# Kernel tuning notes

Measured on AMD Instinct MI355X. Metric: run time of the kernel, lower is better.

The kernel has to match this reference:

```python
import jax, jax.numpy as jnp
import numpy as np
import math

D_MODEL = 1024
N_HEADS = 16
HEAD_DIM = D_MODEL // N_HEADS  # 64
KV_DIM = 4 * HEAD_DIM          # 256
THETA = 10000.0
B, T = 2, 2048


def setup_inputs() -> dict:
    key = jax.random.key(0)
    ks = jax.random.split(key, 14)
    s = lambda k, *sh: jax.random.normal(k, sh, dtype=jnp.float32) * 0.02
    inp = {
        "x": jax.random.normal(ks[0], (B, T, D_MODEL), dtype=jnp.float32),
        "mask": jnp.tril(jnp.ones((T, T), dtype=jnp.int32))[None, None],  # causal [1,1,T,T]
        "Wq": s(ks[1], D_MODEL, D_MODEL), "bq": jnp.zeros((D_MODEL,), jnp.float32),
        "Wkv": s(ks[2], D_MODEL, KV_DIM), "bkv": jnp.zeros((KV_DIM,), jnp.float32),
        "Wk": s(ks[3], KV_DIM, D_MODEL), "bk": jnp.zeros((D_MODEL,), jnp.float32),
        "Wv": s(ks[4], KV_DIM, D_MODEL), "bv": jnp.zeros((D_MODEL,), jnp.float32),
        "Wo": s(ks[5], D_MODEL, D_MODEL), "bo": jnp.zeros((D_MODEL,), jnp.float32),
        "Wkr": s(ks[6], HEAD_DIM, HEAD_DIM),  # decoupled k_rope linear, no bias
    }
    return inp


def _rotate_half(x):
    x1, x2 = jnp.split(x, 2, axis=-1)
    return jnp.concatenate((-x2, x1), axis=-1)


def reference(x, mask, Wq, bq, Wkv, bkv, Wk, bk, Wv, bv, Wo, bo, Wkr):
    Bq, Tq, C = x.shape
    kv = x @ Wkv + bkv                                # [B,T,KV_DIM]
    k = (kv @ Wk + bk).reshape(Bq, Tq, N_HEADS, HEAD_DIM).transpose(0, 2, 1, 3)
    v = (kv @ Wv + bv).reshape(Bq, Tq, N_HEADS, HEAD_DIM).transpose(0, 2, 1, 3)
    q = (x @ Wq + bq).reshape(Bq, Tq, N_HEADS, HEAD_DIM).transpose(0, 2, 1, 3)

    # standard RoPE on q
    inv_freq = 1.0 / (THETA ** (jnp.arange(0, HEAD_DIM, 2, dtype=jnp.float32) / HEAD_DIM))
    t = jnp.arange(Tq, dtype=jnp.float32)
    freqs = t[:, None] * inv_freq[None, :]            # [T, D/2]
    emb = jnp.concatenate((freqs, freqs), axis=-1)    # [T, D]
    q = q * jnp.cos(emb) + _rotate_half(q) * jnp.sin(emb)

    # decoupled position path for k: scale by position index, then linear
    k = (k * t[None, None, :, None]) @ Wkr            # [B,H,T,D]

    attn = jnp.einsum('bhtd,bhsd->bhts', q, k) * (1.0 / math.sqrt(HEAD_DIM))
    attn = jnp.where(mask == 0, -jnp.inf, attn)
    attn = jax.nn.softmax(attn, axis=-1)
    y = jnp.einsum('bhts,bhsd->bhtd', attn, v)
    y = y.transpose(0, 2, 1, 3).reshape(Bq, Tq, C)
    return y @ Wo + bo
```

## Files before the change

### kernel.cpp

```cpp
#include <hip/hip_runtime.h>
#include <hip/hip_bf16.h>
#include <math.h>

typedef __bf16 bf16x8 __attribute__((ext_vector_type(8)));
typedef __bf16 bf16x4 __attribute__((ext_vector_type(4)));
typedef float  f32x4  __attribute__((ext_vector_type(4)));

#define T_SEQ 2048
#define NH    16
#define HD    64
#define DM    1024
#define QSCALE 0.18033688011112043f

__device__ __forceinline__ f32x4 mfma16(bf16x8 a, bf16x8 b, f32x4 c) {
    return __builtin_amdgcn_mfma_f32_16x16x32_bf16(a, b, c, 0, 0, 0);
}

__device__ __forceinline__ void gl2lds(const void* g, void* l) {
    __builtin_amdgcn_global_load_lds(
        (const __attribute__((address_space(1))) void*)g,
        (__attribute__((address_space(3))) void*)l, 16, 0, 0);
}

__device__ __forceinline__ void tsplit_body(const float* __restrict__ in,
                                            __bf16* __restrict__ oh, __bf16* __restrict__ ol,
                                            int K, int N, int n0, int k0, int SPLIT,
                                            float* tile )
{
    const int tid = threadIdx.x;
#pragma unroll
    for (int it = 0; it < 2; ++it) {
        int r = it * 32 + (tid >> 3), c8 = (tid & 7) * 8;
        f32x4 a0 = *(const f32x4*)&in[(size_t)(k0 + r) * N + n0 + c8];
        f32x4 a1 = *(const f32x4*)&in[(size_t)(k0 + r) * N + n0 + c8 + 4];
#pragma unroll
        for (int j = 0; j < 4; ++j) { tile[r * 65 + c8 + j] = a0[j]; tile[r * 65 + c8 + 4 + j] = a1[j]; }
    }
    __syncthreads();
    const int n = tid >> 2, kb = (tid & 3) * 16;
    bf16x8 h0, h1, l0, l1;
#pragma unroll
    for (int j = 0; j < 8; ++j) {
        float v0 = tile[(kb + j) * 65 + n], v1 = tile[(kb + 8 + j) * 65 + n];
        __bf16 hb0 = (__bf16)v0, hb1 = (__bf16)v1;
        h0[j] = hb0; h1[j] = hb1;
        if (SPLIT) { l0[j] = (__bf16)(v0 - (float)hb0); l1[j] = (__bf16)(v1 - (float)hb1); }
    }
    size_t o = (size_t)(n0 + n) * K + k0 + kb;
    *(bf16x8*)&oh[o] = h0; *(bf16x8*)&oh[o + 8] = h1;
    if (SPLIT) { *(bf16x8*)&ol[o] = l0; *(bf16x8*)&ol[o + 8] = l1; }
}

__global__ __launch_bounds__(256)
void prep(const float* __restrict__ x, const float* __restrict__ Wq,
          const float* __restrict__ Wkv, const float* __restrict__ Wv,
          const float* __restrict__ Wo, const float* __restrict__ Wk,
          const float* __restrict__ Wkr, const float* __restrict__ bk,
          __bf16* xh, __bf16* xl, __bf16* Wqt_h, __bf16* Wqt_l,
          __bf16* Wkvt_h, __bf16* Wkvt_l, __bf16* Wvt, __bf16* Wot,
          __bf16* W2th, __bf16* W2tl, float* b2)
{
    __shared__ float tile[64 * 65];
    const int g = blockIdx.x, tid = threadIdx.x;
    if (g < 2048) {
        size_t idx = ((size_t)g * 256 + tid) * 8;
        f32x4 a0 = *(const f32x4*)&x[idx];
        f32x4 a1 = *(const f32x4*)&x[idx + 4];
        bf16x8 h, l;
#pragma unroll
        for (int j = 0; j < 4; ++j) {
            __bf16 h0 = (__bf16)a0[j];
            h[j]     = h0; l[j]     = (__bf16)(a0[j] - (float)h0);
            __bf16 h1 = (__bf16)a1[j];
            h[4 + j] = h1; l[4 + j] = (__bf16)(a1[j] - (float)h1);
        }
        *(bf16x8*)&xh[idx] = h;
        *(bf16x8*)&xl[idx] = l;
    } else if (g < 2304) {
        int i = g - 2048;
        tsplit_body(Wq, Wqt_h, Wqt_l, 1024, 1024, (i & 15) * 64, (i >> 4) * 64, 1, tile);
    } else if (g < 2368) {
        int i = g - 2304;
        tsplit_body(Wkv, Wkvt_h, Wkvt_l, 1024, 256, (i & 3) * 64, (i >> 2) * 64, 1, tile);
    } else if (g < 2432) {
        int i = g - 2368;
        tsplit_body(Wv, Wvt, nullptr, 256, 1024, (i & 15) * 64, (i >> 4) * 64, 0, tile);
    } else if (g < 2688) {
        int i = g - 2432;
        tsplit_body(Wo, Wot, nullptr, 1024, 1024, (i & 15) * 64, (i >> 4) * 64, 0, tile);
    } else {
        int o    = (g - 2688) * 256 + tid;
        int rowk = o >> 10, col = o & 1023;
        int h = col >> 6, d = col & 63;
        float acc = 0.0f;
        if (rowk < 256) {
#pragma unroll 8
            for (int j = 0; j < 64; ++j)
                acc += Wk[(size_t)rowk * DM + h * HD + j] * Wkr[j * HD + d];
            __bf16 hb = (__bf16)acc;
            W2th[(size_t)col * 256 + rowk] = hb;
            W2tl[(size_t)col * 256 + rowk] = (__bf16)(acc - (float)hb);
        } else {
#pragma unroll 8
            for (int j = 0; j < 64; ++j)
                acc += bk[h * HD + j] * Wkr[j * HD + d];
            b2[col] = acc;
        }
    }
}

template <int DUALA, int DUALB, int OUTM, int EPI>
__device__ __forceinline__
void gemm_body(char* smem,
               const __bf16* __restrict__ Ahi, const __bf16* __restrict__ Alo,
               const __bf16* __restrict__ Bhi, const __bf16* __restrict__ Blo,
               const float* __restrict__ bias, void* __restrict__ Cp,
               void* __restrict__ Cp2, int m0, int n0, int N, int K)
{
    const int tid  = threadIdx.x;
    const int w    = tid >> 6;
    const int lane = tid & 63;
    const int l16  = lane & 15;
    const int quad = lane >> 4;
    const int wy   = w >> 1, wx = w & 1;

    f32x4 acc[4][4];
#pragma unroll
    for (int i = 0; i < 4; ++i)
#pragma unroll
        for (int j = 0; j < 4; ++j) acc[i][j] = (f32x4)0.0f;

    auto stage = [&](int k0, int buf) {
        char* bb = smem + buf * 32768;
#pragma unroll
        for (int i = 0; i < 2; ++i) {
            int s = i * 256 + tid, row = s >> 2, c8 = (s & 3) * 8;
            size_t aoff = (size_t)(m0 + row) * K + k0 + c8;
            size_t boff = (size_t)(n0 + row) * K + k0 + c8;
            char*  dst  = bb + (row * 32 + c8) * 2;
            gl2lds(&Ahi[aoff], dst);
            if (DUALA) gl2lds(&Alo[aoff], dst + 8192);
            gl2lds(&Bhi[boff], dst + 16384);
            if (DUALB) gl2lds(&Blo[boff], dst + 24576);
        }
    };

    stage(0, 0);
    const int J = K >> 5;
    for (int j = 0; j < J; ++j) {
        __syncthreads();
        if (j + 1 < J) stage((j + 1) << 5, (j + 1) & 1);

        const __bf16* Ah = (const __bf16*)(smem + (j & 1) * 32768);
        const __bf16* Al = Ah + 4096;
        const __bf16* Bh = Ah + 8192;
        const __bf16* Bl = Ah + 12288;

        bf16x8 bfh[4], bfl[4];
#pragma unroll
        for (int ct = 0; ct < 4; ++ct) {
            bfh[ct] = *(const bf16x8*)&Bh[(wx * 64 + ct * 16 + l16) * 32 + quad * 8];
            if (DUALB) bfl[ct] = *(const bf16x8*)&Bl[(wx * 64 + ct * 16 + l16) * 32 + quad * 8];
        }
#pragma unroll
        for (int mf = 0; mf < 4; ++mf) {
            bf16x8 ah = *(const bf16x8*)&Ah[(wy * 64 + mf * 16 + l16) * 32 + quad * 8];
            bf16x8 al;
            if (DUALA) al = *(const bf16x8*)&Al[(wy * 64 + mf * 16 + l16) * 32 + quad * 8];
#pragma unroll
            for (int ct = 0; ct < 4; ++ct) {
                acc[mf][ct] = mfma16(ah, bfh[ct], acc[mf][ct]);
                if (DUALA) acc[mf][ct] = mfma16(al, bfh[ct], acc[mf][ct]);
                if (DUALB) acc[mf][ct] = mfma16(ah, bfl[ct], acc[mf][ct]);
            }
        }
    }

    float bias_v[4];
#pragma unroll
    for (int ct = 0; ct < 4; ++ct)
        bias_v[ct] = bias ? bias[n0 + wx * 64 + ct * 16 + l16] : 0.0f;

    if (EPI == 1) {
        __bf16* Chi = (__bf16*)Cp;
        __bf16* Clo = (__bf16*)Cp2;
#pragma unroll
        for (int mf = 0; mf < 4; ++mf) {
#pragma unroll
            for (int r = 0; r < 4; ++r) {
                int   m = m0 + wy * 64 + mf * 16 + quad * 4 + r;
                float t = (float)(m & (T_SEQ - 1));
#pragma unroll
                for (int ct = 0; ct < 2; ++ct) {
                    int   d   = ct * 16 + l16;
                    float inv = powf(10000.0f, -(float)d * (1.0f / 32.0f));
                    float sv, cv;
                    sincosf(t * inv, &sv, &cv);
                    float lo = acc[mf][ct][r]     + bias_v[ct];
                    float hi = acc[mf][ct + 2][r] + bias_v[ct + 2];
                    float v0 = (lo * cv - hi * sv) * QSCALE;
                    float v1 = (hi * cv + lo * sv) * QSCALE;
                    size_t i0 = (size_t)m * N + n0 + wx * 64 + d;
                    size_t i1 = i0 + 32;
                    __bf16 h0 = (__bf16)v0, h1 = (__bf16)v1;
                    Chi[i0] = h0; Clo[i0] = (__bf16)(v0 - (float)h0);
                    Chi[i1] = h1; Clo[i1] = (__bf16)(v1 - (float)h1);
                }
            }
        }
    } else if (EPI == 3) {
        __syncthreads();
        __bf16* vt = (__bf16*)(smem + w * 9216);
#pragma unroll
        for (int mf = 0; mf < 4; ++mf)
#pragma unroll
            for (int ct = 0; ct < 4; ++ct)
#pragma unroll
                for (int r = 0; r < 4; ++r)
                    vt[(ct * 16 + l16) * 72 + mf * 16 + quad * 4 + r] =
                        (__bf16)(acc[mf][ct][r] + bias_v[ct]);
        const int bb   = m0 >> 11;
        const int head = (n0 + wx * 64) >> 6;
        const int bh   = bb * 16 + head;
        __bf16* out    = (__bf16*)Cp;
        size_t  gbase  = ((size_t)(bh * 64 + lane)) * T_SEQ + (m0 & (T_SEQ - 1)) + wy * 64;
#pragma unroll
        for (int j8 = 0; j8 < 8; ++j8)
            *(bf16x8*)&out[gbase + j8 * 8] = *(const bf16x8*)&vt[lane * 72 + j8 * 8];
    } else {
#pragma unroll
        for (int mf = 0; mf < 4; ++mf) {
#pragma unroll
            for (int r = 0; r < 4; ++r) {
                int   m     = m0 + wy * 64 + mf * 16 + quad * 4 + r;
                float scale = (EPI == 2) ? (float)(m & (T_SEQ - 1)) : 1.0f;
#pragma unroll
                for (int ct = 0; ct < 4; ++ct) {
                    float  v   = (acc[mf][ct][r] + bias_v[ct]) * scale;
                    size_t idx = (size_t)m * N + n0 + wx * 64 + ct * 16 + l16;
                    if (OUTM == 1)      ((float*)Cp)[idx]  = v;
                    else if (OUTM == 0) ((__bf16*)Cp)[idx] = (__bf16)v;
                    else {
                        __bf16 hb = (__bf16)v;
                        ((__bf16*)Cp)[idx]  = hb;
                        ((__bf16*)Cp2)[idx] = (__bf16)(v - (float)hb);
                    }
                }
            }
        }
    }
}

__global__ __launch_bounds__(256)
void gemm_qkv(const __bf16* xh, const __bf16* xl,
              const __bf16* Wqt_h, const __bf16* Wqt_l, const float* bq,
              __bf16* qhi, __bf16* qlo,
              const __bf16* Wkvt_h, const __bf16* Wkvt_l, const float* bkv,
              __bf16* kvhi, __bf16* kvlo)
{
    __shared__ __attribute__((aligned(16))) char smem[65536];
    const int m0 = blockIdx.y * 128;
    if (blockIdx.x < 2)
        gemm_body<1, 1, 2, 0>(smem, xh, xl, Wkvt_h, Wkvt_l, bkv, kvhi, kvlo,
                              m0, blockIdx.x * 128, 256, 1024);
    else
        gemm_body<1, 1, 2, 1>(smem, xh, xl, Wqt_h, Wqt_l, bq, qhi, qlo,
                              m0, (blockIdx.x - 2) * 128, 1024, 1024);
}

__global__ __launch_bounds__(256)
void gemm_kv2(const __bf16* kvhi, const __bf16* kvlo,
              const __bf16* W2th, const __bf16* W2tl, const float* b2,
              __bf16* khi, __bf16* klo,
              const __bf16* Wvt, const float* bv, __bf16* vtg)
{
    __shared__ __attribute__((aligned(16))) char smem[65536];
    const int m0 = blockIdx.y * 128;
    if (blockIdx.x < 8)
        gemm_body<1, 1, 2, 2>(smem, kvhi, kvlo, W2th, W2tl, b2, khi, klo,
                              m0, blockIdx.x * 128, 1024, 256);
    else
        gemm_body<1, 0, 0, 3>(smem, kvhi, kvlo, Wvt, Wvt, bv, vtg, nullptr,
                              m0, (blockIdx.x - 8) * 128, 1024, 256);
}

__global__ __launch_bounds__(256)
void gemm_o(const __bf16* ybb, const __bf16* Wot, const float* bo, float* out)
{
    __shared__ __attribute__((aligned(16))) char smem[65536];
    gemm_body<0, 0, 1, 0>(smem, ybb, ybb, Wot, Wot, bo, out, nullptr,
                          blockIdx.y * 128, blockIdx.x * 128, 1024, 1024);
}

#define KSP 72
#define PSP 72
__global__ __launch_bounds__(256, 2)
void attn_v5(const __bf16* __restrict__ qhi, const __bf16* __restrict__ qlo,
             const __bf16* __restrict__ khi, const __bf16* __restrict__ klo,
             const __bf16* __restrict__ vtg, __bf16* __restrict__ yb)
{
    __shared__ __attribute__((aligned(16))) __bf16 Kh2[2][64 * KSP];
    __shared__ __attribute__((aligned(16))) __bf16 Kl2[2][64 * KSP];
    __shared__ __attribute__((aligned(16))) __bf16 Vt2[2][64 * KSP];
    __shared__ __attribute__((aligned(16))) __bf16 Pw[4][2][16 * PSP];

    const int tid  = threadIdx.x;
    const int w    = tid >> 6;
    const int lane = tid & 63;
    const int l16  = lane & 15;
    const int quad = lane >> 4;

    const int g  = blockIdx.x;
    const int bh = g & 31, a = g >> 5;
    const int tile = (a < 8) ? (15 - 2 * a) : (2 * (a - 8));
    const int b = bh >> 4, h = bh & 15;
    const int q0 = tile * 128;

    bf16x8 qh[2][2], ql[2][2];
#pragma unroll
    for (int f = 0; f < 2; ++f) {
        const int    qrow = q0 + 64 * f + 16 * w + l16;
        const size_t qoff = (size_t)(b * T_SEQ + qrow) * DM + h * HD;
#pragma unroll
        for (int s = 0; s < 2; ++s) {
            qh[f][s] = *(const bf16x8*)&qhi[qoff + s * 32 + quad * 8];
            ql[f][s] = *(const bf16x8*)&qlo[qoff + s * 32 + quad * 8];
        }
    }

    f32x4 o[2][4];
#pragma unroll
    for (int f = 0; f < 2; ++f)
#pragma unroll
        for (int i = 0; i < 4; ++i) o[f][i] = (f32x4)0.0f;
    float m_i[2] = {-1e30f, -1e30f}, l_i[2] = {0.f, 0.f};

    const int srow = tid >> 3, sc8 = (tid & 7) * 8;
    bf16x8 kr[2], lr[2], vr[2];

#pragma unroll
    for (int it = 0; it < 2; ++it) {
        int    r  = it * 32 + srow;
        size_t gk = (size_t)(b * T_SEQ + r) * DM + h * HD + sc8;
        kr[it] = *(const bf16x8*)&khi[gk];
        lr[it] = *(const bf16x8*)&klo[gk];
        vr[it] = *(const bf16x8*)&vtg[(size_t)(bh * HD + r) * T_SEQ + sc8];
    }
#pragma unroll
    for (int it = 0; it < 2; ++it) {
        int r = it * 32 + srow;
        *(bf16x8*)&Kh2[0][r * KSP + sc8] = kr[it];
        *(bf16x8*)&Kl2[0][r * KSP + sc8] = lr[it];
        *(bf16x8*)&Vt2[0][r * KSP + sc8] = vr[it];
    }

    const int jmax = q0 + 64;
    for (int j0 = 0; j0 <= jmax; j0 += 64) {
        const int  cur  = (j0 >> 6) & 1;
        const bool act0 = (j0 <= q0);
        const bool pre  = (j0 + 64 <= jmax);
        __syncthreads();

        if (pre) {
#pragma unroll
            for (int it = 0; it < 2; ++it) {
                int    r  = it * 32 + srow;
                size_t gk = (size_t)(b * T_SEQ + j0 + 64 + r) * DM + h * HD + sc8;
                kr[it] = *(const bf16x8*)&khi[gk];
                lr[it] = *(const bf16x8*)&klo[gk];
                vr[it] = *(const bf16x8*)&vtg[(size_t)(bh * HD + r) * T_SEQ + j0 + 64 + sc8];
            }
        }

        const __bf16* Kh = Kh2[cur];
        const __bf16* Kl = Kl2[cur];
        const __bf16* Vt = Vt2[cur];

        f32x4 sa[2][4];
#pragma unroll
        for (int f = 0; f < 2; ++f)
#pragma unroll
            for (int i = 0; i < 4; ++i) sa[f][i] = (f32x4)0.0f;
#pragma unroll
        for (int s = 0; s < 2; ++s) {
#pragma unroll
            for (int kc = 0; kc < 4; ++kc) {
                bf16x8 kh = *(const bf16x8*)&Kh[(kc * 16 + l16) * KSP + s * 32 + quad * 8];
                bf16x8 kv = *(const bf16x8*)&Kl[(kc * 16 + l16) * KSP + s * 32 + quad * 8];
                sa[1][kc] = mfma16(kh, qh[1][s], sa[1][kc]);
                sa[1][kc] = mfma16(kv, qh[1][s], sa[1][kc]);
                sa[1][kc] = mfma16(kh, ql[1][s], sa[1][kc]);
                if (act0) {
                    sa[0][kc] = mfma16(kh, qh[0][s], sa[0][kc]);
                    sa[0][kc] = mfma16(kv, qh[0][s], sa[0][kc]);
                    sa[0][kc] = mfma16(kh, ql[0][s], sa[0][kc]);
                }
            }
        }

#pragma unroll
        for (int f = 0; f < 2; ++f) {
            if (f == 0 && !act0) continue;
            const int  qrow = q0 + 64 * f + 16 * w + l16;
            const bool need = (j0 + 63 > q0 + 64 * f + 16 * w);
            if (need) {
#pragma unroll
                for (int kc = 0; kc < 4; ++kc)
#pragma unroll
                    for (int r = 0; r < 4; ++r)
                        if (j0 + kc * 16 + quad * 4 + r > qrow) sa[f][kc][r] = -1e30f;
            }
            float mx = -1e30f;
#pragma unroll
            for (int kc = 0; kc < 4; ++kc)
#pragma unroll
                for (int r = 0; r < 4; ++r) mx = fmaxf(mx, sa[f][kc][r]);
            mx = fmaxf(mx, __shfl_xor(mx, 16));
            mx = fmaxf(mx, __shfl_xor(mx, 32));
            float mn    = fmaxf(fmaxf(m_i[f], mx), -1e20f);
            float alpha = exp2f(m_i[f] - mn);
            m_i[f] = mn;
            float rs = 0.f;
            __bf16* pw = &Pw[w][f][0];
#pragma unroll
            for (int kc = 0; kc < 4; ++kc) {
                float p0 = exp2f(sa[f][kc][0] - mn);
                float p1 = exp2f(sa[f][kc][1] - mn);
                float p2 = exp2f(sa[f][kc][2] - mn);
                float p3 = exp2f(sa[f][kc][3] - mn);
                rs += (p0 + p1) + (p2 + p3);
                bf16x4 pk = { (__bf16)p0, (__bf16)p1, (__bf16)p2, (__bf16)p3 };
                *(bf16x4*)&pw[l16 * PSP + kc * 16 + quad * 4] = pk;
            }
            rs += __shfl_xor(rs, 16);
            rs += __shfl_xor(rs, 32);
            l_i[f] = l_i[f] * alpha + rs;
#pragma unroll
            for (int dc = 0; dc < 4; ++dc) o[f][dc] *= alpha;
        }

#pragma unroll
        for (int s = 0; s < 2; ++s) {
            bf16x8 pb1 = *(const bf16x8*)&Pw[w][1][l16 * PSP + s * 32 + quad * 8];
            bf16x8 pb0;
            if (act0) pb0 = *(const bf16x8*)&Pw[w][0][l16 * PSP + s * 32 + quad * 8];
#pragma unroll
            for (int dc = 0; dc < 4; ++dc) {
                bf16x8 va = *(const bf16x8*)&Vt[(dc * 16 + l16) * KSP + s * 32 + quad * 8];
                o[1][dc] = mfma16(va, pb1, o[1][dc]);
                if (act0) o[0][dc] = mfma16(va, pb0, o[0][dc]);
            }
        }

        if (pre) {
            __bf16* nKh = Kh2[cur ^ 1];
            __bf16* nKl = Kl2[cur ^ 1];
            __bf16* nVt = Vt2[cur ^ 1];
#pragma unroll
            for (int it = 0; it < 2; ++it) {
                int r = it * 32 + srow;
                *(bf16x8*)&nKh[r * KSP + sc8] = kr[it];
                *(bf16x8*)&nKl[r * KSP + sc8] = lr[it];
                *(bf16x8*)&nVt[r * KSP + sc8] = vr[it];
            }
        }
    }

#pragma unroll
    for (int f = 0; f < 2; ++f) {
        float   invl = 1.0f / l_i[f];
        __bf16* pw   = &Pw[w][f][0];
#pragma unroll
        for (int dc = 0; dc < 4; ++dc) {
            bf16x4 ov = { (__bf16)(o[f][dc][0] * invl), (__bf16)(o[f][dc][1] * invl),
                          (__bf16)(o[f][dc][2] * invl), (__bf16)(o[f][dc][3] * invl) };
            *(bf16x4*)&pw[l16 * PSP + dc * 16 + quad * 4] = ov;
        }
        const int qrl  = lane >> 2;
        const int dch  = (lane & 3) * 16;
        const int qrow = q0 + 64 * f + 16 * w + qrl;
        const __bf16* src = &pw[qrl * PSP + dch];
        __bf16*       dst = &yb[(size_t)(b * T_SEQ + qrow) * DM + h * HD + dch];
        *(bf16x8*)dst       = *(const bf16x8*)src;
        *(bf16x8*)(dst + 8) = *(const bf16x8*)(src + 8);
    }
}

extern "C" void kernel_launch(void* const* d_in, const int* in_sizes, int n_in,
                              void* d_out, int out_size, void* d_ws, size_t ws_size,
                              hipStream_t stream)
{
    (void)in_sizes; (void)n_in; (void)out_size; (void)ws_size;

    const float* x   = (const float*)d_in[0];
    const float* Wq  = (const float*)d_in[2];
    const float* bq  = (const float*)d_in[3];
    const float* Wkv = (const float*)d_in[4];
    const float* bkv = (const float*)d_in[5];
    const float* Wk  = (const float*)d_in[6];
    const float* bk  = (const float*)d_in[7];
    const float* Wv  = (const float*)d_in[8];
    const float* bv  = (const float*)d_in[9];
    const float* Wo  = (const float*)d_in[10];
    const float* bo  = (const float*)d_in[11];
    const float* Wkr = (const float*)d_in[12];

    const int    BT = 2 * T_SEQ;
    const size_t MB = 1024 * 1024;
    char* base = (char*)d_ws;

    __bf16* xhi    = (__bf16*)(base +  0 * MB);
    __bf16* xlo    = (__bf16*)(base +  8 * MB);
    __bf16* qhi    = (__bf16*)(base + 16 * MB);
    __bf16* qlo    = (__bf16*)(base + 24 * MB);
    __bf16* Wqt_h  = (__bf16*)(base + 32 * MB);
    __bf16* Wqt_l  = (__bf16*)(base + 34 * MB);
    __bf16* Wkvt_h = (__bf16*)(base + 36 * MB);
    __bf16* Wkvt_l = (__bf16*)(base + 37 * MB);
    __bf16* kvhi   = (__bf16*)(base + 38 * MB);
    __bf16* kvlo   = (__bf16*)(base + 40 * MB);
    __bf16* W2t_h  = (__bf16*)(base + 42 * MB);
    __bf16* W2t_l  = (__bf16*)(base + 42 * MB + 512 * 1024);
    __bf16* Wvt    = (__bf16*)(base + 43 * MB);
    __bf16* Wot    = (__bf16*)(base + 43 * MB + 512 * 1024);
    float*  b2     = (float*) (base + 45 * MB + 512 * 1024);
    __bf16* vtg    = (__bf16*)(base +  8 * MB);
    __bf16* ybb    = (__bf16*)(base +  0 * MB);
    __bf16* khi    = (__bf16*)d_out;
    __bf16* klo    = (__bf16*)d_out + (size_t)BT * DM;

    dim3 blk(256);
    prep<<<3716, blk, 0, stream>>>(x, Wq, Wkv, Wv, Wo, Wk, Wkr, bk,
                                   xhi, xlo, Wqt_h, Wqt_l, Wkvt_h, Wkvt_l,
                                   Wvt, Wot, W2t_h, W2t_l, b2);
    gemm_qkv<<<dim3(10, 32), blk, 0, stream>>>(xhi, xlo, Wqt_h, Wqt_l, bq, qhi, qlo,
                                               Wkvt_h, Wkvt_l, bkv, kvhi, kvlo);
    gemm_kv2<<<dim3(16, 32), blk, 0, stream>>>(kvhi, kvlo, W2t_h, W2t_l, b2,
                                               khi, klo, Wvt, bv, vtg);
    attn_v5<<<512, blk, 0, stream>>>(qhi, qlo, khi, klo, vtg, ybb);
    gemm_o<<<dim3(8, 32), blk, 0, stream>>>(ybb, Wot, bo, (float*)d_out);
}
```

Before: 283.4 us.

## Restructure causal attention blocks into paired 64-row tiles for load balance

Each attention block now handles two 64-row query tiles in sequence, tile 31-a and then tile a, instead of one 128-row tile carrying two fragments. Pairing a long tile with a short one gives every block the same causal workload, and each warp now keeps a single fragment's state. The cost is that K/V blocks are reloaded for the second phase, and the 128-row tile's sharing of each K/V load across two query fragments is lost, so LDS reuse per load drops.

```diff
diff --git a/kernel.cpp b/kernel.cpp
--- a/kernel.cpp
+++ b/kernel.cpp
@@ -295,14 +295,14 @@
 #define KSP 72
 #define PSP 72
 __global__ __launch_bounds__(256, 2)
-void attn_v5(const __bf16* __restrict__ qhi, const __bf16* __restrict__ qlo,
+void attn_v7(const __bf16* __restrict__ qhi, const __bf16* __restrict__ qlo,
              const __bf16* __restrict__ khi, const __bf16* __restrict__ klo,
              const __bf16* __restrict__ vtg, __bf16* __restrict__ yb)
 {
     __shared__ __attribute__((aligned(16))) __bf16 Kh2[2][64 * KSP];
     __shared__ __attribute__((aligned(16))) __bf16 Kl2[2][64 * KSP];
     __shared__ __attribute__((aligned(16))) __bf16 Vt2[2][64 * KSP];
-    __shared__ __attribute__((aligned(16))) __bf16 Pw[4][2][16 * PSP];
+    __shared__ __attribute__((aligned(16))) __bf16 Pw[4][16 * PSP];
 
     const int tid  = threadIdx.x;
     const int w    = tid >> 6;
@@ -312,177 +312,161 @@
 
     const int g  = blockIdx.x;
     const int bh = g & 31, a = g >> 5;
-    const int tile = (a < 8) ? (15 - 2 * a) : (2 * (a - 8));
-    const int b = bh >> 4, h = bh & 15;
-    const int q0 = tile * 128;
-
-    bf16x8 qh[2][2], ql[2][2];
-#pragma unroll
-    for (int f = 0; f < 2; ++f) {
-        const int    qrow = q0 + 64 * f + 16 * w + l16;
-        const size_t qoff = (size_t)(b * T_SEQ + qrow) * DM + h * HD;
-#pragma unroll
-        for (int s = 0; s < 2; ++s) {
-            qh[f][s] = *(const bf16x8*)&qhi[qoff + s * 32 + quad * 8];
-            ql[f][s] = *(const bf16x8*)&qlo[qoff + s * 32 + quad * 8];
-        }
-    }
-
-    f32x4 o[2][4];
-#pragma unroll
-    for (int f = 0; f < 2; ++f)
-#pragma unroll
-        for (int i = 0; i < 4; ++i) o[f][i] = (f32x4)0.0f;
-    float m_i[2] = {-1e30f, -1e30f}, l_i[2] = {0.f, 0.f};
+    const int b  = bh >> 4, h = bh & 15;
 
     const int srow = tid >> 3, sc8 = (tid & 7) * 8;
-    bf16x8 kr[2], lr[2], vr[2];
-
-#pragma unroll
-    for (int it = 0; it < 2; ++it) {
-        int    r  = it * 32 + srow;
-        size_t gk = (size_t)(b * T_SEQ + r) * DM + h * HD + sc8;
-        kr[it] = *(const bf16x8*)&khi[gk];
-        lr[it] = *(const bf16x8*)&klo[gk];
-        vr[it] = *(const bf16x8*)&vtg[(size_t)(bh * HD + r) * T_SEQ + sc8];
-    }
-#pragma unroll
-    for (int it = 0; it < 2; ++it) {
-        int r = it * 32 + srow;
-        *(bf16x8*)&Kh2[0][r * KSP + sc8] = kr[it];
-        *(bf16x8*)&Kl2[0][r * KSP + sc8] = lr[it];
-        *(bf16x8*)&Vt2[0][r * KSP + sc8] = vr[it];
-    }
-
-    const int jmax = q0 + 64;
-    for (int j0 = 0; j0 <= jmax; j0 += 64) {
-        const int  cur  = (j0 >> 6) & 1;
-        const bool act0 = (j0 <= q0);
-        const bool pre  = (j0 + 64 <= jmax);
+
+    for (int ph = 0; ph < 2; ++ph) {
+        const int u  = ph ? a : (31 - a);
+        const int q0 = u * 64;
+
+        bf16x8 qh[2], ql[2];
+        {
+            const int    qr   = q0 + 16 * w + l16;
+            const size_t qoff = (size_t)(b * T_SEQ + qr) * DM + h * HD;
+#pragma unroll
+            for (int s = 0; s < 2; ++s) {
+                qh[s] = *(const bf16x8*)&qhi[qoff + s * 32 + quad * 8];
+                ql[s] = *(const bf16x8*)&qlo[qoff + s * 32 + quad * 8];
+            }
+        }
+
+        f32x4 o[4];
+#pragma unroll
+        for (int i = 0; i < 4; ++i) o[i] = (f32x4)0.0f;
+        float m_i = -1e30f, l_i = 0.f;
+
+        bf16x8 kr[2], lr[2], vr[2];
+#pragma unroll
+        for (int it = 0; it < 2; ++it) {
+            int    r  = it * 32 + srow;
+            size_t gk = (size_t)(b * T_SEQ + r) * DM + h * HD + sc8;
+            kr[it] = *(const bf16x8*)&khi[gk];
+            lr[it] = *(const bf16x8*)&klo[gk];
+            vr[it] = *(const bf16x8*)&vtg[(size_t)(bh * HD + r) * T_SEQ + sc8];
+        }
         __syncthreads();
-
-        if (pre) {
-#pragma unroll
-            for (int it = 0; it < 2; ++it) {
-                int    r  = it * 32 + srow;
-                size_t gk = (size_t)(b * T_SEQ + j0 + 64 + r) * DM + h * HD + sc8;
-                kr[it] = *(const bf16x8*)&khi[gk];
-                lr[it] = *(const bf16x8*)&klo[gk];
-                vr[it] = *(const bf16x8*)&vtg[(size_t)(bh * HD + r) * T_SEQ + j0 + 64 + sc8];
-            }
-        }
-
-        const __bf16* Kh = Kh2[cur];
-        const __bf16* Kl = Kl2[cur];
-        const __bf16* Vt = Vt2[cur];
-
-        f32x4 sa[2][4];
-#pragma unroll
-        for (int f = 0; f < 2; ++f)
-#pragma unroll
-            for (int i = 0; i < 4; ++i) sa[f][i] = (f32x4)0.0f;
-#pragma unroll
-        for (int s = 0; s < 2; ++s) {
-#pragma unroll
-            for (int kc = 0; kc < 4; ++kc) {
-                bf16x8 kh = *(const bf16x8*)&Kh[(kc * 16 + l16) * KSP + s * 32 + quad * 8];
-                bf16x8 kv = *(const bf16x8*)&Kl[(kc * 16 + l16) * KSP + s * 32 + quad * 8];
-                sa[1][kc] = mfma16(kh, qh[1][s], sa[1][kc]);
-                sa[1][kc] = mfma16(kv, qh[1][s], sa[1][kc]);
-                sa[1][kc] = mfma16(kh, ql[1][s], sa[1][kc]);
-                if (act0) {
-                    sa[0][kc] = mfma16(kh, qh[0][s], sa[0][kc]);
-                    sa[0][kc] = mfma16(kv, qh[0][s], sa[0][kc]);
-                    sa[0][kc] = mfma16(kh, ql[0][s], sa[0][kc]);
+#pragma unroll
+        for (int it = 0; it < 2; ++it) {
+            int r = it * 32 + srow;
+            *(bf16x8*)&Kh2[0][r * KSP + sc8] = kr[it];
+            *(bf16x8*)&Kl2[0][r * KSP + sc8] = lr[it];
+            *(bf16x8*)&Vt2[0][r * KSP + sc8] = vr[it];
+        }
+
+        for (int j0 = 0; j0 <= q0; j0 += 64) {
+            const int  cur = (j0 >> 6) & 1;
+            const bool pre = (j0 + 64 <= q0);
+            __syncthreads();
+
+            if (pre) {
+#pragma unroll
+                for (int it = 0; it < 2; ++it) {
+                    int    r  = it * 32 + srow;
+                    size_t gk = (size_t)(b * T_SEQ + j0 + 64 + r) * DM + h * HD + sc8;
+                    kr[it] = *(const bf16x8*)&khi[gk];
+                    lr[it] = *(const bf16x8*)&klo[gk];
+                    vr[it] = *(const bf16x8*)&vtg[(size_t)(bh * HD + r) * T_SEQ + j0 + 64 + sc8];
                 }
             }
-        }
-
-#pragma unroll
-        for (int f = 0; f < 2; ++f) {
-            if (f == 0 && !act0) continue;
-            const int  qrow = q0 + 64 * f + 16 * w + l16;
-            const bool need = (j0 + 63 > q0 + 64 * f + 16 * w);
+
+            const __bf16* Kh = Kh2[cur];
+            const __bf16* Kl = Kl2[cur];
+            const __bf16* Vt = Vt2[cur];
+
+            f32x4 sa[4];
+#pragma unroll
+            for (int i = 0; i < 4; ++i) sa[i] = (f32x4)0.0f;
+#pragma unroll
+            for (int s = 0; s < 2; ++s) {
+#pragma unroll
+                for (int kc = 0; kc < 4; ++kc) {
+                    bf16x8 kh = *(const bf16x8*)&Kh[(kc * 16 + l16) * KSP + s * 32 + quad * 8];
+                    bf16x8 kv = *(const bf16x8*)&Kl[(kc * 16 + l16) * KSP + s * 32 + quad * 8];
+                    sa[kc] = mfma16(kh, qh[s], sa[kc]);
+                    sa[kc] = mfma16(kv, qh[s], sa[kc]);
+                    sa[kc] = mfma16(kh, ql[s], sa[kc]);
+                }
+            }
+
+            const int  qr   = q0 + 16 * w + l16;
+            const bool need = (j0 + 63 > q0 + 16 * w);
             if (need) {
 #pragma unroll
                 for (int kc = 0; kc < 4; ++kc)
 #pragma unroll
                     for (int r = 0; r < 4; ++r)
-                        if (j0 + kc * 16 + quad * 4 + r > qrow) sa[f][kc][r] = -1e30f;
+                        if (j0 + kc * 16 + quad * 4 + r > qr) sa[kc][r] = -1e30f;
             }
             float mx = -1e30f;
 #pragma unroll
             for (int kc = 0; kc < 4; ++kc)
 #pragma unroll
-                for (int r = 0; r < 4; ++r) mx = fmaxf(mx, sa[f][kc][r]);
+                for (int r = 0; r < 4; ++r) mx = fmaxf(mx, sa[kc][r]);
             mx = fmaxf(mx, __shfl_xor(mx, 16));
             mx = fmaxf(mx, __shfl_xor(mx, 32));
-            float mn    = fmaxf(fmaxf(m_i[f], mx), -1e20f);
-            float alpha = exp2f(m_i[f] - mn);
-            m_i[f] = mn;
+            float mn    = fmaxf(fmaxf(m_i, mx), -1e20f);
+            float alpha = exp2f(m_i - mn);
+            m_i = mn;
             float rs = 0.f;
-            __bf16* pw = &Pw[w][f][0];
+            __bf16* pw = &Pw[w][0];
 #pragma unroll
             for (int kc = 0; kc < 4; ++kc) {
-                float p0 = exp2f(sa[f][kc][0] - mn);
-                float p1 = exp2f(sa[f][kc][1] - mn);
-                float p2 = exp2f(sa[f][kc][2] - mn);
-                float p3 = exp2f(sa[f][kc][3] - mn);
+                float p0 = exp2f(sa[kc][0] - mn);
+                float p1 = exp2f(sa[kc][1] - mn);
+                float p2 = exp2f(sa[kc][2] - mn);
+                float p3 = exp2f(sa[kc][3] - mn);
                 rs += (p0 + p1) + (p2 + p3);
                 bf16x4 pk = { (__bf16)p0, (__bf16)p1, (__bf16)p2, (__bf16)p3 };
                 *(bf16x4*)&pw[l16 * PSP + kc * 16 + quad * 4] = pk;
             }
             rs += __shfl_xor(rs, 16);
             rs += __shfl_xor(rs, 32);
-            l_i[f] = l_i[f] * alpha + rs;
-#pragma unroll
-            for (int dc = 0; dc < 4; ++dc) o[f][dc] *= alpha;
-        }
-
-#pragma unroll
-        for (int s = 0; s < 2; ++s) {
-            bf16x8 pb1 = *(const bf16x8*)&Pw[w][1][l16 * PSP + s * 32 + quad * 8];
-            bf16x8 pb0;
-            if (act0) pb0 = *(const bf16x8*)&Pw[w][0][l16 * PSP + s * 32 + quad * 8];
+            l_i = l_i * alpha + rs;
+#pragma unroll
+            for (int dc = 0; dc < 4; ++dc) o[dc] *= alpha;
+
+#pragma unroll
+            for (int s = 0; s < 2; ++s) {
+                bf16x8 pb = *(const bf16x8*)&pw[l16 * PSP + s * 32 + quad * 8];
+#pragma unroll
+                for (int dc = 0; dc < 4; ++dc) {
+                    bf16x8 va = *(const bf16x8*)&Vt[(dc * 16 + l16) * KSP + s * 32 + quad * 8];
+                    o[dc] = mfma16(va, pb, o[dc]);
+                }
+            }
+
+            if (pre) {
+                __bf16* nKh = Kh2[cur ^ 1];
+                __bf16* nKl = Kl2[cur ^ 1];
+                __bf16* nVt = Vt2[cur ^ 1];
+#pragma unroll
+                for (int it = 0; it < 2; ++it) {
+                    int r = it * 32 + srow;
+                    *(bf16x8*)&nKh[r * KSP + sc8] = kr[it];
+                    *(bf16x8*)&nKl[r * KSP + sc8] = lr[it];
+                    *(bf16x8*)&nVt[r * KSP + sc8] = vr[it];
+                }
+            }
+        }
+
+        {
+            float   invl = 1.0f / l_i;
+            __bf16* pw   = &Pw[w][0];
 #pragma unroll
             for (int dc = 0; dc < 4; ++dc) {
-                bf16x8 va = *(const bf16x8*)&Vt[(dc * 16 + l16) * KSP + s * 32 + quad * 8];
-                o[1][dc] = mfma16(va, pb1, o[1][dc]);
-                if (act0) o[0][dc] = mfma16(va, pb0, o[0][dc]);
-            }
-        }
-
-        if (pre) {
-            __bf16* nKh = Kh2[cur ^ 1];
-            __bf16* nKl = Kl2[cur ^ 1];
-            __bf16* nVt = Vt2[cur ^ 1];
-#pragma unroll
-            for (int it = 0; it < 2; ++it) {
-                int r = it * 32 + srow;
-                *(bf16x8*)&nKh[r * KSP + sc8] = kr[it];
-                *(bf16x8*)&nKl[r * KSP + sc8] = lr[it];
-                *(bf16x8*)&nVt[r * KSP + sc8] = vr[it];
-            }
-        }
-    }
-
-#pragma unroll
-    for (int f = 0; f < 2; ++f) {
-        float   invl = 1.0f / l_i[f];
-        __bf16* pw   = &Pw[w][f][0];
-#pragma unroll
-        for (int dc = 0; dc < 4; ++dc) {
-            bf16x4 ov = { (__bf16)(o[f][dc][0] * invl), (__bf16)(o[f][dc][1] * invl),
-                          (__bf16)(o[f][dc][2] * invl), (__bf16)(o[f][dc][3] * invl) };
-            *(bf16x4*)&pw[l16 * PSP + dc * 16 + quad * 4] = ov;
-        }
-        const int qrl  = lane >> 2;
-        const int dch  = (lane & 3) * 16;
-        const int qrow = q0 + 64 * f + 16 * w + qrl;
-        const __bf16* src = &pw[qrl * PSP + dch];
-        __bf16*       dst = &yb[(size_t)(b * T_SEQ + qrow) * DM + h * HD + dch];
-        *(bf16x8*)dst       = *(const bf16x8*)src;
-        *(bf16x8*)(dst + 8) = *(const bf16x8*)(src + 8);
+                bf16x4 ov = { (__bf16)(o[dc][0] * invl), (__bf16)(o[dc][1] * invl),
+                              (__bf16)(o[dc][2] * invl), (__bf16)(o[dc][3] * invl) };
+                *(bf16x4*)&pw[l16 * PSP + dc * 16 + quad * 4] = ov;
+            }
+            const int qrl  = lane >> 2;
+            const int dch  = (lane & 3) * 16;
+            const int qrow = q0 + 16 * w + qrl;
+            const __bf16* src = &pw[qrl * PSP + dch];
+            __bf16*       dst = &yb[(size_t)(b * T_SEQ + qrow) * DM + h * HD + dch];
+            *(bf16x8*)dst       = *(const bf16x8*)src;
+            *(bf16x8*)(dst + 8) = *(const bf16x8*)(src + 8);
+        }
     }
 }
 
@@ -537,6 +521,6 @@
                                                Wkvt_h, Wkvt_l, bkv, kvhi, kvlo);
     gemm_kv2<<<dim3(16, 32), blk, 0, stream>>>(kvhi, kvlo, W2t_h, W2t_l, b2,
                                                khi, klo, Wvt, bv, vtg);
-    attn_v5<<<512, blk, 0, stream>>>(qhi, qlo, khi, klo, vtg, ybb);
+    attn_v7<<<512, blk, 0, stream>>>(qhi, qlo, khi, klo, vtg, ybb);
     gemm_o<<<dim3(8, 32), blk, 0, stream>>>(ybb, Wot, bo, (float*)d_out);
 }
```

Result: faster. 257.7 us (-9.0%).
